# Optimization experiments

Hardware: AMD Instinct MI355X
Metric: run time of the kernel (lower is better)

## Reference

```python
import jax, jax.numpy as jnp
import numpy as np

N_NODES = 100000
IMPROVED_FILL = 2.0  # improved=True in GCNConv -> self-loop weight 2.0


def setup_inputs() -> dict:
    key = jax.random.key(0)
    k1, k2, k3 = jax.random.split(key, 3)
    x = jax.random.normal(k1, (N_NODES, 128), dtype=jnp.float32)
    edge_index = jax.random.randint(k2, (2, 640000), 0, N_NODES, dtype=jnp.int64)
    # Glorot-style init like PyG's GCNConv weight
    W = jax.random.normal(k3, (128, 128), dtype=jnp.float32) * (1.0 / np.sqrt(128))
    b = jnp.zeros((128,), dtype=jnp.float32)
    return {"x": x, "edge_index": edge_index, "W": W, "b": b}


def reference(x, edge_index, W, b):
    N = x.shape[0]
    E = edge_index.shape[1]
    # --- gcn_norm with improved self-loops (fill value 2.0) ---
    loop = jnp.arange(N, dtype=edge_index.dtype)
    row = jnp.concatenate([edge_index[0], loop])  # source nodes
    col = jnp.concatenate([edge_index[1], loop])  # target nodes
    ew = jnp.concatenate([jnp.ones((E,), x.dtype), jnp.full((N,), IMPROVED_FILL, x.dtype)])
    deg = jax.ops.segment_sum(ew, col, num_segments=N)
    dinv = jnp.where(deg > 0, jax.lax.rsqrt(deg), 0.0)
    norm = dinv[row] * ew * dinv[col]  # [E+N]
    # --- linear transform then normalized scatter-add aggregation ---
    xW = x @ W  # [N, out]
    msgs = norm[:, None] * xW[row]  # [E+N, out]
    out = jax.ops.segment_sum(msgs, col, num_segments=N)
    return out + b
```

## Files before the change

kernel.cpp:

```cpp
#include <hip/hip_runtime.h>

#define GCN_N 100000
#define GCN_E 640000
#define GCN_F 128
#define NPB  32
#define CAP  32
#define ZROW 100000

typedef __attribute__((ext_vector_type(8))) short bf16x8;
typedef __attribute__((ext_vector_type(4))) float f32x4;
typedef __attribute__((ext_vector_type(8))) unsigned short ushort8;

__device__ inline unsigned short f2bf(float f) {
    unsigned u = __float_as_uint(f);
    return (unsigned short)((u + 0x7fff + ((u >> 16) & 1)) >> 16);
}
__device__ inline float bflo(unsigned u) { return __uint_as_float(u << 16); }
__device__ inline float bfhi(unsigned u) { return __uint_as_float(u & 0xffff0000u); }

__global__ void fill_xs(const int* __restrict__ rows, const int* __restrict__ cols,
                        int* __restrict__ cnt, int* __restrict__ ell,
                        const float* __restrict__ x, ushort* __restrict__ xs,
                        const float* __restrict__ W,
                        ushort* __restrict__ wfh, ushort* __restrict__ wfl) {
    int blk = blockIdx.x;
    int t = threadIdx.x;
    if (blk < 2500) {
        int e = blk * 256 + t;
        int c = cols[e], r = rows[e];
        int k = atomicAdd(&cnt[c], 1);
        if (k < CAP) ell[(size_t)c * CAP + k] = r;
        return;
    }
    if (blk < 15000) {
        int i = (blk - 2500) * 256 + t;
        float4 v = ((const float4*)x)[i];
        ushort4 o;
        o.x = f2bf(v.x); o.y = f2bf(v.y);
        o.z = f2bf(v.z); o.w = f2bf(v.w);
        ((ushort4*)xs)[i] = o;
        return;
    }
    if (blk == 15000) {
        if (t < 32) ((ushort4*)xs)[(size_t)ZROW * 32 + t] = make_ushort4(0, 0, 0, 0);
        return;
    }
    int p    = blk - 15001;
    int pi   = p * 4 + (t >> 6);
    int lane = t & 63;
    int kt = pi >> 3, nt = pi & 7;
    int kr   = kt * 32 + ((lane >> 4) * 8);
    int ncol = nt * 16 + (lane & 15);
    ushort8 hv, lv;
#pragma unroll
    for (int j = 0; j < 8; ++j) {
        float w = W[(size_t)(kr + j) * GCN_F + ncol];
        unsigned short h = f2bf(w);
        hv[j] = h;
        lv[j] = f2bf(w - bflo((unsigned)h));
    }
    size_t fo = (size_t)(kt * 8 + nt) * 64 + lane;
    ((ushort8*)wfh)[fo] = hv;
    ((ushort8*)wfl)[fo] = lv;
}

__global__ __launch_bounds__(256) void gcn_fused(
        const ushort* __restrict__ xs, const int* __restrict__ cnt,
        const int* __restrict__ ell, const ushort* __restrict__ wfh,
        const ushort* __restrict__ wfl, const float* __restrict__ b,
        float* __restrict__ out) {
    __shared__ ushort Ah[NPB * GCN_F];
    __shared__ ushort Al[NPB * GCN_F];
    __shared__ int    sell[NPB * CAP];
    __shared__ int    scnt[NPB];
    int t = threadIdx.x;
    int row0 = blockIdx.x * NPB;

    if (t < NPB) scnt[t] = cnt[row0 + t];
    __syncthreads();

    for (int i = t; i < NPB * CAP; i += 256) {
        int rr = i >> 5, kk = i & (CAP - 1);
        int v = ell[(size_t)(row0 + rr) * CAP + kk];
        int dg = scnt[rr]; if (dg > CAP) dg = CAP;
        sell[i] = (kk < dg) ? v : ZROW;
    }
    __syncthreads();

    int lane = t & 63;
    int wv   = t >> 6;

    {
        const unsigned* xs2 = (const unsigned*)xs;
        for (int q = 0; q < 8; ++q) {
            int rr = wv * 8 + q;
            int c  = row0 + rr;
            const int* sp = &sell[rr * CAP];
            int4 m0 = *(const int4*)sp;
            int4 m1 = *(const int4*)(sp + 4);
            int4 m2 = *(const int4*)(sp + 8);
            int4 m3 = *(const int4*)(sp + 12);
            unsigned s0 = xs2[c * 64 + lane];
            unsigned v[16];
            int cq[16];
            v[ 0] = xs2[m0.x * 64 + lane]; cq[ 0] = cnt[m0.x];
            v[ 1] = xs2[m0.y * 64 + lane]; cq[ 1] = cnt[m0.y];
            v[ 2] = xs2[m0.z * 64 + lane]; cq[ 2] = cnt[m0.z];
            v[ 3] = xs2[m0.w * 64 + lane]; cq[ 3] = cnt[m0.w];
            v[ 4] = xs2[m1.x * 64 + lane]; cq[ 4] = cnt[m1.x];
            v[ 5] = xs2[m1.y * 64 + lane]; cq[ 5] = cnt[m1.y];
            v[ 6] = xs2[m1.z * 64 + lane]; cq[ 6] = cnt[m1.z];
            v[ 7] = xs2[m1.w * 64 + lane]; cq[ 7] = cnt[m1.w];
            v[ 8] = xs2[m2.x * 64 + lane]; cq[ 8] = cnt[m2.x];
            v[ 9] = xs2[m2.y * 64 + lane]; cq[ 9] = cnt[m2.y];
            v[10] = xs2[m2.z * 64 + lane]; cq[10] = cnt[m2.z];
            v[11] = xs2[m2.w * 64 + lane]; cq[11] = cnt[m2.w];
            v[12] = xs2[m3.x * 64 + lane]; cq[12] = cnt[m3.x];
            v[13] = xs2[m3.y * 64 + lane]; cq[13] = cnt[m3.y];
            v[14] = xs2[m3.z * 64 + lane]; cq[14] = cnt[m3.z];
            v[15] = xs2[m3.w * 64 + lane]; cq[15] = cnt[m3.w];
            int dc = scnt[rr];
            float dic = rsqrtf(2.0f + (float)dc);
            float sw  = 2.0f * dic;
            float ax = sw * bflo(s0);
            float ay = sw * bfhi(s0);
#pragma unroll
            for (int k = 0; k < 16; ++k) {
                float dm = rsqrtf(2.0f + (float)cq[k]);
                ax = fmaf(dm, bflo(v[k]), ax);
                ay = fmaf(dm, bfhi(v[k]), ay);
            }
            int deg = dc > CAP ? CAP : dc;
            if (deg > 16) {
                for (int k = 16; k < deg; ++k) {
                    int m = sp[k];
                    unsigned u = xs2[m * 64 + lane];
                    float dm = rsqrtf(2.0f + (float)cnt[m]);
                    ax = fmaf(dm, bflo(u), ax);
                    ay = fmaf(dm, bfhi(u), ay);
                }
            }
            float axd = dic * ax, ayd = dic * ay;
            unsigned short hx = f2bf(axd), hy = f2bf(ayd);
            unsigned short lx = f2bf(axd - bflo((unsigned)hx));
            unsigned short ly = f2bf(ayd - bflo((unsigned)hy));
            unsigned off = (unsigned)rr * 256 + (((unsigned)lane * 4) ^ (((unsigned)(rr & 7)) << 4));
            *(unsigned*)((char*)Ah + off) = ((unsigned)hy << 16) | hx;
            *(unsigned*)((char*)Al + off) = ((unsigned)ly << 16) | lx;
        }
    }
    __syncthreads();

    int lrow  = lane & 15;
    int lhalf = lane >> 4;
    f32x4 acc[2][2];
#pragma unroll
    for (int m = 0; m < 2; ++m)
#pragma unroll
        for (int n = 0; n < 2; ++n) acc[m][n] = (f32x4)0.f;

    const bf16x8* whp = (const bf16x8*)wfh;
    const bf16x8* wlp = (const bf16x8*)wfl;
    int nt0 = wv * 2;

#pragma unroll
    for (int kt = 0; kt < 4; ++kt) {
        unsigned kb = ((unsigned)(kt * 64 + lhalf * 16)) ^ (((unsigned)(lane & 7)) << 4);
        unsigned o0 = (unsigned)lrow * 256 + kb;
        bf16x8 ah[2], al[2], wh[2], wl[2];
        ah[0] = *(const bf16x8*)((const char*)Ah + o0);
        ah[1] = *(const bf16x8*)((const char*)Ah + o0 + 4096);
        al[0] = *(const bf16x8*)((const char*)Al + o0);
        al[1] = *(const bf16x8*)((const char*)Al + o0 + 4096);
        wh[0] = whp[(kt * 8 + nt0) * 64 + lane];
        wh[1] = whp[(kt * 8 + nt0 + 1) * 64 + lane];
        wl[0] = wlp[(kt * 8 + nt0) * 64 + lane];
        wl[1] = wlp[(kt * 8 + nt0 + 1) * 64 + lane];
#pragma unroll
        for (int m = 0; m < 2; ++m)
#pragma unroll
            for (int n = 0; n < 2; ++n) {
                acc[m][n] = __builtin_amdgcn_mfma_f32_16x16x32_bf16(ah[m], wh[n], acc[m][n], 0, 0, 0);
                acc[m][n] = __builtin_amdgcn_mfma_f32_16x16x32_bf16(ah[m], wl[n], acc[m][n], 0, 0, 0);
                acc[m][n] = __builtin_amdgcn_mfma_f32_16x16x32_bf16(al[m], wh[n], acc[m][n], 0, 0, 0);
            }
    }

    float b0 = b[wv * 32 + lrow];
    float b1 = b[wv * 32 + 16 + lrow];
#pragma unroll
    for (int m = 0; m < 2; ++m)
#pragma unroll
        for (int n = 0; n < 2; ++n) {
            int col = wv * 32 + n * 16 + lrow;
            float bb = n ? b1 : b0;
#pragma unroll
            for (int j = 0; j < 4; ++j) {
                int r = row0 + m * 16 + lhalf * 4 + j;
                out[(size_t)r * GCN_F + col] = acc[m][n][j] + bb;
            }
        }
}

extern "C" void kernel_launch(void* const* d_in, const int* in_sizes, int n_in,
                              void* d_out, int out_size, void* d_ws, size_t ws_size,
                              hipStream_t stream) {
    const float* x  = (const float*)d_in[0];
    const int*   ei = (const int*)d_in[1];
    const float* W  = (const float*)d_in[2];
    const float* b  = (const float*)d_in[3];
    float* out = (float*)d_out;

    const int N = GCN_N, E = GCN_E;
    const int* rows = ei;
    const int* cols = ei + E;

    char*   ws  = (char*)d_ws;
    int*    cnt = (int*)(ws + 0);
    int*    ell = (int*)(ws + 400384);
    ushort* xs  = (ushort*)(ws + 13200384);
    ushort* wfh = (ushort*)(ws + 38800640);
    ushort* wfl = (ushort*)(ws + 38833408);

    hipMemsetAsync(cnt, 0, (size_t)(N + 1) * sizeof(int), stream);
    fill_xs<<<15009, 256, 0, stream>>>(rows, cols, cnt, ell, x, xs, W, wfh, wfl);
    gcn_fused<<<N / NPB, 256, 0, stream>>>(xs, cnt, ell, wfh, wfl, b, out);
}
```

Baseline: 194.9 us.

## Precompute dinv, pre-fill ELL with zero-row sentinel, use scalar neighbor indices

```diff
diff --git a/kernel.cpp b/kernel.cpp
--- a/kernel.cpp
+++ b/kernel.cpp
@@ -18,11 +18,16 @@
 __device__ inline float bflo(unsigned u) { return __uint_as_float(u << 16); }
 __device__ inline float bfhi(unsigned u) { return __uint_as_float(u & 0xffff0000u); }
 
-__global__ void fill_xs(const int* __restrict__ rows, const int* __restrict__ cols,
-                        int* __restrict__ cnt, int* __restrict__ ell,
-                        const float* __restrict__ x, ushort* __restrict__ xs,
-                        const float* __restrict__ W,
-                        ushort* __restrict__ wfh, ushort* __restrict__ wfl) {
+__global__ void init_ell(int* __restrict__ ell) {
+    int i = blockIdx.x * 256 + threadIdx.x;
+    ((int4*)ell)[i] = make_int4(ZROW, ZROW, ZROW, ZROW);
+}
+
+__global__ void fill_all(const int* __restrict__ rows, const int* __restrict__ cols,
+                         int* __restrict__ cnt, int* __restrict__ ell,
+                         const float* __restrict__ x, ushort* __restrict__ xs,
+                         const float* __restrict__ W,
+                         ushort* __restrict__ wfh, ushort* __restrict__ wfl) {
     int blk = blockIdx.x;
     int t = threadIdx.x;
     if (blk < 2500) {
@@ -64,29 +69,20 @@
     ((ushort8*)wfl)[fo] = lv;
 }
 
+__global__ void dinv_k(const int* __restrict__ cnt, float* __restrict__ dinv) {
+    int i = blockIdx.x * 256 + threadIdx.x;
+    if (i <= GCN_N) dinv[i] = rsqrtf(2.0f + (float)cnt[i]);
+}
+
 __global__ __launch_bounds__(256) void gcn_fused(
         const ushort* __restrict__ xs, const int* __restrict__ cnt,
-        const int* __restrict__ ell, const ushort* __restrict__ wfh,
-        const ushort* __restrict__ wfl, const float* __restrict__ b,
-        float* __restrict__ out) {
+        const int* __restrict__ ell, const float* __restrict__ dinv,
+        const ushort* __restrict__ wfh, const ushort* __restrict__ wfl,
+        const float* __restrict__ b, float* __restrict__ out) {
     __shared__ ushort Ah[NPB * GCN_F];
     __shared__ ushort Al[NPB * GCN_F];
-    __shared__ int    sell[NPB * CAP];
-    __shared__ int    scnt[NPB];
     int t = threadIdx.x;
     int row0 = blockIdx.x * NPB;
-
-    if (t < NPB) scnt[t] = cnt[row0 + t];
-    __syncthreads();
-
-    for (int i = t; i < NPB * CAP; i += 256) {
-        int rr = i >> 5, kk = i & (CAP - 1);
-        int v = ell[(size_t)(row0 + rr) * CAP + kk];
-        int dg = scnt[rr]; if (dg > CAP) dg = CAP;
-        sell[i] = (kk < dg) ? v : ZROW;
-    }
-    __syncthreads();
-
     int lane = t & 63;
     int wv   = t >> 6;
 
@@ -95,49 +91,53 @@
         for (int q = 0; q < 8; ++q) {
             int rr = wv * 8 + q;
             int c  = row0 + rr;
-            const int* sp = &sell[rr * CAP];
-            int4 m0 = *(const int4*)sp;
-            int4 m1 = *(const int4*)(sp + 4);
-            int4 m2 = *(const int4*)(sp + 8);
-            int4 m3 = *(const int4*)(sp + 12);
+            const int4* ep = (const int4*)(ell + (size_t)c * CAP);
+            int4 m0 = ep[0];
+            int4 m1 = ep[1];
+            int4 m2 = ep[2];
+            int4 m3 = ep[3];
+            int dc = cnt[c];
+            float dic = dinv[c];
             unsigned s0 = xs2[c * 64 + lane];
+            int sm[16];
+            sm[ 0] = __builtin_amdgcn_readfirstlane(m0.x);
+            sm[ 1] = __builtin_amdgcn_readfirstlane(m0.y);
+            sm[ 2] = __builtin_amdgcn_readfirstlane(m0.z);
+            sm[ 3] = __builtin_amdgcn_readfirstlane(m0.w);
+            sm[ 4] = __builtin_amdgcn_readfirstlane(m1.x);
+            sm[ 5] = __builtin_amdgcn_readfirstlane(m1.y);
+            sm[ 6] = __builtin_amdgcn_readfirstlane(m1.z);
+            sm[ 7] = __builtin_amdgcn_readfirstlane(m1.w);
+            sm[ 8] = __builtin_amdgcn_readfirstlane(m2.x);
+            sm[ 9] = __builtin_amdgcn_readfirstlane(m2.y);
+            sm[10] = __builtin_amdgcn_readfirstlane(m2.z);
+            sm[11] = __builtin_amdgcn_readfirstlane(m2.w);
+            sm[12] = __builtin_amdgcn_readfirstlane(m3.x);
+            sm[13] = __builtin_amdgcn_readfirstlane(m3.y);
+            sm[14] = __builtin_amdgcn_readfirstlane(m3.z);
+            sm[15] = __builtin_amdgcn_readfirstlane(m3.w);
             unsigned v[16];
-            int cq[16];
-            v[ 0] = xs2[m0.x * 64 + lane]; cq[ 0] = cnt[m0.x];
-            v[ 1] = xs2[m0.y * 64 + lane]; cq[ 1] = cnt[m0.y];
-            v[ 2] = xs2[m0.z * 64 + lane]; cq[ 2] = cnt[m0.z];
-            v[ 3] = xs2[m0.w * 64 + lane]; cq[ 3] = cnt[m0.w];
-            v[ 4] = xs2[m1.x * 64 + lane]; cq[ 4] = cnt[m1.x];
-            v[ 5] = xs2[m1.y * 64 + lane]; cq[ 5] = cnt[m1.y];
-            v[ 6] = xs2[m1.z * 64 + lane]; cq[ 6] = cnt[m1.z];
-            v[ 7] = xs2[m1.w * 64 + lane]; cq[ 7] = cnt[m1.w];
-            v[ 8] = xs2[m2.x * 64 + lane]; cq[ 8] = cnt[m2.x];
-            v[ 9] = xs2[m2.y * 64 + lane]; cq[ 9] = cnt[m2.y];
-            v[10] = xs2[m2.z * 64 + lane]; cq[10] = cnt[m2.z];
-            v[11] = xs2[m2.w * 64 + lane]; cq[11] = cnt[m2.w];
-            v[12] = xs2[m3.x * 64 + lane]; cq[12] = cnt[m3.x];
-            v[13] = xs2[m3.y * 64 + lane]; cq[13] = cnt[m3.y];
-            v[14] = xs2[m3.z * 64 + lane]; cq[14] = cnt[m3.z];
-            v[15] = xs2[m3.w * 64 + lane]; cq[15] = cnt[m3.w];
-            int dc = scnt[rr];
-            float dic = rsqrtf(2.0f + (float)dc);
-            float sw  = 2.0f * dic;
-            float ax = sw * bflo(s0);
-            float ay = sw * bfhi(s0);
+            float dm[16];
 #pragma unroll
             for (int k = 0; k < 16; ++k) {
-                float dm = rsqrtf(2.0f + (float)cq[k]);
-                ax = fmaf(dm, bflo(v[k]), ax);
-                ay = fmaf(dm, bfhi(v[k]), ay);
+                v[k]  = xs2[sm[k] * 64 + lane];
+                dm[k] = dinv[sm[k]];
+            }
+            float ax = 2.0f * dic * bflo(s0);
+            float ay = 2.0f * dic * bfhi(s0);
+#pragma unroll
+            for (int k = 0; k < 16; ++k) {
+                ax = fmaf(dm[k], bflo(v[k]), ax);
+                ay = fmaf(dm[k], bfhi(v[k]), ay);
             }
             int deg = dc > CAP ? CAP : dc;
             if (deg > 16) {
                 for (int k = 16; k < deg; ++k) {
-                    int m = sp[k];
+                    int m = __builtin_amdgcn_readfirstlane(((const int*)ep)[k]);
                     unsigned u = xs2[m * 64 + lane];
-                    float dm = rsqrtf(2.0f + (float)cnt[m]);
-                    ax = fmaf(dm, bflo(u), ax);
-                    ay = fmaf(dm, bfhi(u), ay);
+                    float dmm = dinv[m];
+                    ax = fmaf(dmm, bflo(u), ax);
+                    ay = fmaf(dmm, bfhi(u), ay);
                 }
             }
             float axd = dic * ax, ayd = dic * ay;
@@ -215,14 +215,17 @@
     const int* rows = ei;
     const int* cols = ei + E;
 
-    char*   ws  = (char*)d_ws;
-    int*    cnt = (int*)(ws + 0);
-    int*    ell = (int*)(ws + 400384);
-    ushort* xs  = (ushort*)(ws + 13200384);
-    ushort* wfh = (ushort*)(ws + 38800640);
-    ushort* wfl = (ushort*)(ws + 38833408);
+    char*   ws   = (char*)d_ws;
+    int*    cnt  = (int*)(ws + 0);
+    int*    ell  = (int*)(ws + 400384);
+    ushort* xs   = (ushort*)(ws + 13200384);
+    ushort* wfh  = (ushort*)(ws + 38800640);
+    ushort* wfl  = (ushort*)(ws + 38833408);
+    float*  dinv = (float*)(ws + 38866176);
 
     hipMemsetAsync(cnt, 0, (size_t)(N + 1) * sizeof(int), stream);
-    fill_xs<<<15009, 256, 0, stream>>>(rows, cols, cnt, ell, x, xs, W, wfh, wfl);
-    gcn_fused<<<N / NPB, 256, 0, stream>>>(xs, cnt, ell, wfh, wfl, b, out);
-}
+    init_ell<<<3125, 256, 0, stream>>>(ell);
+    fill_all<<<15009, 256, 0, stream>>>(rows, cols, cnt, ell, x, xs, W, wfh, wfl);
+    dinv_k<<<392, 256, 0, stream>>>(cnt, dinv);
+    gcn_fused<<<N / NPB, 256, 0, stream>>>(xs, cnt, ell, dinv, wfh, wfl, b, out);
+}
```

After: 187.9 us. -3.6%, faster.
